# Kernel optimization log

Hardware: AMD Instinct MI355X
Metric: run time of the kernel (lower is better)

## Reference

```python
import jax, jax.numpy as jnp
import numpy as np

H, W, N = 256, 256, 1024
CHOLESKY_BOUND = jnp.array([0.5, 0.0, 0.5], dtype=jnp.float32)


def setup_inputs() -> dict:
    key = jax.random.key(0)
    k1, k2, k3 = jax.random.split(key, 3)
    return {
        "xyz": jax.random.normal(k1, (N, 2), dtype=jnp.float32),        # pre-tanh positions
        "cholesky": jax.random.uniform(k2, (N, 3), dtype=jnp.float32),  # l1, l2, l3
        "opacity": jnp.ones((N, 1), dtype=jnp.float32),
        "features_dc": jax.random.uniform(k3, (N, 3), dtype=jnp.float32),
    }


def reference(xyz, cholesky, opacity, features_dc):
    # project_gaussians_2d: map tanh(xyz) in [-1,1] to pixel coords
    means = jnp.tanh(xyz)                                  # [N,2]
    cx = 0.5 * W * (means[:, 0] + 1.0)                     # [N]
    cy = 0.5 * H * (means[:, 1] + 1.0)
    # Sigma = L L^T with L = [[l1,0],[l2,l3]]; conic = Sigma^{-1}
    L = cholesky + CHOLESKY_BOUND
    l1, l2, l3 = L[:, 0], L[:, 1], L[:, 2]
    a = l1 * l1                                            # Sigma_xx
    b = l1 * l2                                            # Sigma_xy
    c = l2 * l2 + l3 * l3                                  # Sigma_yy
    det = a * c - b * b
    conic_a = c / det                                      # conic xx
    conic_b = -b / det                                     # conic xy
    conic_c = a / det                                      # conic yy
    # rasterize_gaussians_sum: accumulate c_i * o_i * exp(-0.5 d^T conic d) per pixel
    px = (jnp.arange(W, dtype=jnp.float32) + 0.5)          # pixel centers
    py = (jnp.arange(H, dtype=jnp.float32) + 0.5)
    gx, gy = jnp.meshgrid(px, py)                          # [H,W]
    dx = gx.reshape(-1)[None, :] - cx[:, None]             # [N,HW]
    dy = gy.reshape(-1)[None, :] - cy[:, None]             # [N,HW]
    sigma = 0.5 * (conic_a[:, None] * dx * dx + conic_c[:, None] * dy * dy) \
            + conic_b[:, None] * dx * dy                   # [N,HW]
    w = jnp.exp(-sigma)                                    # gaussian weight per (gaussian, pixel)
    feat = features_dc * opacity                           # [N,3]
    img = jnp.einsum('np,nc->pc', w, feat)                 # [HW,3] summed splat
    img = jnp.clip(img, 0.0, 1.0)
    return img.reshape(1, H, W, 3).transpose(0, 3, 1, 2)   # [1,3,H,W]
```

## Files before the change

### kernel.cpp

```cpp
#include <hip/hip_runtime.h>

#define W_IMG 256
#define H_IMG 256
#define NPTS  1024
#define SIG_CUT 15.0f

__global__ __launch_bounds__(256) void gsplat_tiled(
    const float* __restrict__ xyz,
    const float* __restrict__ chol,
    const float* __restrict__ opac,
    const float* __restrict__ feat,
    float* __restrict__ out)
{
    __shared__ float4 sp4[NPTS * 2];
    __shared__ int scnt;

    const int tid = threadIdx.x;
    const int tx0 = (blockIdx.x & 15) << 4;
    const int ty0 = (blockIdx.x >> 4) << 4;

    if (tid == 0) scnt = 0;
    __syncthreads();

    const float LOG2E     = 1.4426950408889634f;
    const float TWO_LOG2E = 2.8853900817779268f;

    for (int i = tid; i < NPTS; i += 256) {
        float e0 = exp2f(TWO_LOG2E * xyz[2 * i + 0]);
        float e1 = exp2f(TWO_LOG2E * xyz[2 * i + 1]);
        float mx = 1.0f - 2.0f * __builtin_amdgcn_rcpf(e0 + 1.0f);
        float my = 1.0f - 2.0f * __builtin_amdgcn_rcpf(e1 + 1.0f);
        float cx = 0.5f * (float)W_IMG * (mx + 1.0f);
        float cy = 0.5f * (float)H_IMG * (my + 1.0f);

        float l1 = chol[3 * i + 0] + 0.5f;
        float l2 = chol[3 * i + 1];
        float l3 = chol[3 * i + 2] + 0.5f;
        float a = l1 * l1;
        float b = l1 * l2;
        float c = fmaf(l2, l2, l3 * l3);

        float rx = sqrtf(2.0f * SIG_CUT * a);
        float ry = sqrtf(2.0f * SIG_CUT * c);

        bool hit = (cx >= (float)tx0 - rx) && (cx <= (float)(tx0 + 16) + rx) &&
                   (cy >= (float)ty0 - ry) && (cy <= (float)(ty0 + 16) + ry);
        if (hit) {
            float det = fmaf(a, c, -b * b);
            float inv = __builtin_amdgcn_rcpf(det);
            float o = opac[i];
            int slot = atomicAdd(&scnt, 1);
            sp4[2 * slot + 0] = make_float4(cx, cy, -0.5f * c * inv * LOG2E, b * inv * LOG2E);
            sp4[2 * slot + 1] = make_float4(-0.5f * a * inv * LOG2E,
                                            feat[3 * i + 0] * o,
                                            feat[3 * i + 1] * o,
                                            feat[3 * i + 2] * o);
        }
    }
    __syncthreads();
    const int n = scnt;

    const int x = tx0 + (tid & 15);
    const int y = ty0 + (tid >> 4);
    const float px = (float)x + 0.5f;
    const float py = (float)y + 0.5f;

    float r = 0.0f, g = 0.0f, bl = 0.0f;
    #pragma unroll 4
    for (int j = 0; j < n; ++j) {
        float4 q0 = sp4[2 * j + 0];
        float4 q1 = sp4[2 * j + 1];
        float dx = px - q0.x;
        float dy = py - q0.y;
        float t  = fmaf(q0.z, dx, q0.w * dy);
        float s  = fmaf(dx, t, (q1.x * dy) * dy);
        float w  = exp2f(s);
        r  = fmaf(w, q1.y, r);
        g  = fmaf(w, q1.z, g);
        bl = fmaf(w, q1.w, bl);
    }

    const int p = y * W_IMG + x;
    out[0 * H_IMG * W_IMG + p] = fminf(fmaxf(r,  0.0f), 1.0f);
    out[1 * H_IMG * W_IMG + p] = fminf(fmaxf(g,  0.0f), 1.0f);
    out[2 * H_IMG * W_IMG + p] = fminf(fmaxf(bl, 0.0f), 1.0f);
}

extern "C" void kernel_launch(void* const* d_in, const int* in_sizes, int n_in,
                              void* d_out, int out_size, void* d_ws, size_t ws_size,
                              hipStream_t stream) {
    const float* xyz  = (const float*)d_in[0];
    const float* chol = (const float*)d_in[1];
    const float* opac = (const float*)d_in[2];
    const float* feat = (const float*)d_in[3];
    float* out = (float*)d_out;
    (void)in_sizes; (void)n_in; (void)out_size; (void)d_ws; (void)ws_size;

    gsplat_tiled<<<(W_IMG / 16) * (H_IMG / 16), 256, 0, stream>>>(xyz, chol, opac, feat, out);
}
```

Baseline: 62.42 us.

## Split per-Gaussian preprocessing into a separate prep kernel writing to workspace

Moves the tanh projection, conic inversion and culling-radius computation out of the render kernel into a small prep kernel that runs once per Gaussian and stores packed float4 records in the workspace. Each of the 256 tile blocks then only reads the bounds record, tests overlap, and copies precomputed records into shared memory. This removes redundant per-tile transcendental and divide work, at the cost of a second kernel launch and a global-memory round trip.

```diff
diff --git a/kernel.cpp b/kernel.cpp
--- a/kernel.cpp
+++ b/kernel.cpp
@@ -5,11 +5,51 @@
 #define NPTS  1024
 #define SIG_CUT 15.0f
 
-__global__ __launch_bounds__(256) void gsplat_tiled(
+
+__global__ __launch_bounds__(256) void gsplat_prep(
     const float* __restrict__ xyz,
     const float* __restrict__ chol,
     const float* __restrict__ opac,
     const float* __restrict__ feat,
+    float4* __restrict__ ws)
+{
+    const int i = blockIdx.x * 256 + threadIdx.x;
+    const float LOG2E     = 1.4426950408889634f;
+    const float TWO_LOG2E = 2.8853900817779268f;
+
+    float2 xy = ((const float2*)xyz)[i];
+    float e0 = exp2f(TWO_LOG2E * xy.x);
+    float e1 = exp2f(TWO_LOG2E * xy.y);
+    float mx = 1.0f - 2.0f * __builtin_amdgcn_rcpf(e0 + 1.0f);
+    float my = 1.0f - 2.0f * __builtin_amdgcn_rcpf(e1 + 1.0f);
+    float cx = 0.5f * (float)W_IMG * (mx + 1.0f);
+    float cy = 0.5f * (float)H_IMG * (my + 1.0f);
+
+    float l1 = chol[3 * i + 0] + 0.5f;
+    float l2 = chol[3 * i + 1];
+    float l3 = chol[3 * i + 2] + 0.5f;
+    float a = l1 * l1;
+    float b = l1 * l2;
+    float c = fmaf(l2, l2, l3 * l3);
+
+    float rx = sqrtf(2.0f * SIG_CUT * a);
+    float ry = sqrtf(2.0f * SIG_CUT * c);
+
+    float det = fmaf(a, c, -b * b);
+    float inv = __builtin_amdgcn_rcpf(det);
+    float o = opac[i];
+
+    ws[i] = make_float4(cx, cy, rx, ry);
+    ws[NPTS + 2 * i + 0] = make_float4(-0.5f * c * inv * LOG2E,
+                                        b * inv * LOG2E,
+                                        -0.5f * a * inv * LOG2E, 0.0f);
+    ws[NPTS + 2 * i + 1] = make_float4(feat[3 * i + 0] * o,
+                                       feat[3 * i + 1] * o,
+                                       feat[3 * i + 2] * o, 0.0f);
+}
+
+__global__ __launch_bounds__(256) void gsplat_render(
+    const float4* __restrict__ ws,
     float* __restrict__ out)
 {
     __shared__ float4 sp4[NPTS * 2];
@@ -22,39 +62,20 @@
     if (tid == 0) scnt = 0;
     __syncthreads();
 
-    const float LOG2E     = 1.4426950408889634f;
-    const float TWO_LOG2E = 2.8853900817779268f;
+    const float xlo = (float)tx0,      xhi = (float)(tx0 + 16);
+    const float ylo = (float)ty0,      yhi = (float)(ty0 + 16);
 
+    #pragma unroll 4
     for (int i = tid; i < NPTS; i += 256) {
-        float e0 = exp2f(TWO_LOG2E * xyz[2 * i + 0]);
-        float e1 = exp2f(TWO_LOG2E * xyz[2 * i + 1]);
-        float mx = 1.0f - 2.0f * __builtin_amdgcn_rcpf(e0 + 1.0f);
-        float my = 1.0f - 2.0f * __builtin_amdgcn_rcpf(e1 + 1.0f);
-        float cx = 0.5f * (float)W_IMG * (mx + 1.0f);
-        float cy = 0.5f * (float)H_IMG * (my + 1.0f);
-
-        float l1 = chol[3 * i + 0] + 0.5f;
-        float l2 = chol[3 * i + 1];
-        float l3 = chol[3 * i + 2] + 0.5f;
-        float a = l1 * l1;
-        float b = l1 * l2;
-        float c = fmaf(l2, l2, l3 * l3);
-
-        float rx = sqrtf(2.0f * SIG_CUT * a);
-        float ry = sqrtf(2.0f * SIG_CUT * c);
-
-        bool hit = (cx >= (float)tx0 - rx) && (cx <= (float)(tx0 + 16) + rx) &&
-                   (cy >= (float)ty0 - ry) && (cy <= (float)(ty0 + 16) + ry);
+        float4 q = ws[i];
+        bool hit = (q.x >= xlo - q.z) && (q.x <= xhi + q.z) &&
+                   (q.y >= ylo - q.w) && (q.y <= yhi + q.w);
         if (hit) {
-            float det = fmaf(a, c, -b * b);
-            float inv = __builtin_amdgcn_rcpf(det);
-            float o = opac[i];
+            float4 qa = ws[NPTS + 2 * i + 0];
+            float4 qb = ws[NPTS + 2 * i + 1];
             int slot = atomicAdd(&scnt, 1);
-            sp4[2 * slot + 0] = make_float4(cx, cy, -0.5f * c * inv * LOG2E, b * inv * LOG2E);
-            sp4[2 * slot + 1] = make_float4(-0.5f * a * inv * LOG2E,
-                                            feat[3 * i + 0] * o,
-                                            feat[3 * i + 1] * o,
-                                            feat[3 * i + 2] * o);
+            sp4[2 * slot + 0] = make_float4(q.x, q.y, qa.x, qa.y);
+            sp4[2 * slot + 1] = make_float4(qa.z, qb.x, qb.y, qb.z);
         }
     }
     __syncthreads();
@@ -94,7 +115,9 @@
     const float* opac = (const float*)d_in[2];
     const float* feat = (const float*)d_in[3];
     float* out = (float*)d_out;
-    (void)in_sizes; (void)n_in; (void)out_size; (void)d_ws; (void)ws_size;
+    float4* ws = (float4*)d_ws;
+    (void)in_sizes; (void)n_in; (void)out_size; (void)ws_size;
 
-    gsplat_tiled<<<(W_IMG / 16) * (H_IMG / 16), 256, 0, stream>>>(xyz, chol, opac, feat, out);
+    gsplat_prep<<<NPTS / 256, 256, 0, stream>>>(xyz, chol, opac, feat, ws);
+    gsplat_render<<<(W_IMG / 16) * (H_IMG / 16), 256, 0, stream>>>(ws, out);
 }
```

After: 62.90 us. No clear change (+0.8%).
